# Optimization experiments

Hardware: AMD Instinct MI355X
Metric: run time of the kernel (lower is better)

The kernel has to match this reference:

```python
import jax, jax.numpy as jnp
from jax import lax
import numpy as np

N, D = 1024, 100000
K, SELECT_N = 20, 256  # select_n = int(N * split) = int(1024 * 0.25)


def setup_inputs() -> dict:
    key = jax.random.key(0)
    k1, k2 = jax.random.split(key)
    inp = jax.random.normal(k1, (N, D), dtype=jnp.float32)
    indices = jax.random.randint(k2, (K, SELECT_N), 0, N, dtype=jnp.int32)
    return {"inp": inp, "indices": indices}


def reference(inp, indices):
    # For each of k bagging rounds: gather select_n random rows, max over rows.
    # scan over k keeps the peak intermediate at [select_n, D] instead of [k, select_n, D].
    def step(_, idx):
        return None, jnp.max(inp[idx], axis=0)  # [D]

    _, maxes = lax.scan(step, None, indices)   # [k, D]
    return jnp.mean(maxes, axis=0, keepdims=True)  # [1, D]
```

## Files before the change

### kernel.cpp

```cpp
#include <hip/hip_runtime.h>


#define N_ROWS   1024
#define D_COLS   100000
#define K_ROUNDS 20
#define SEL_N    256
#define NIDX     (K_ROUNDS * SEL_N)
#define CPB      16
#define NT       (D_COLS / CPB)
#define BLOCK    640
#define GRID     256
#define WAVES    10
#define RNDS_PW  (K_ROUNDS / WAVES)
#define NEG_INF  (-3.402823466e+38f)

template<int CTRL>
__device__ __forceinline__ float dpp_shr_max(float x) {
    const int xi = __float_as_int(x);
    const int sh = __builtin_amdgcn_update_dpp(xi, xi, CTRL, 0xF, 0xF, false);
    return fmaxf(x, __int_as_float(sh));
}
#define ROW_SHR4 0x114
#define ROW_SHR8 0x118

__device__ __forceinline__ void async_cp16(const float* g, float* l) {
    __builtin_amdgcn_global_load_lds(
        (const __attribute__((address_space(1))) unsigned int*)g,
        (__attribute__((address_space(3))) unsigned int*)l,
        16, 0, 0);
}

__device__ __forceinline__ void stage_tile(const float* __restrict__ inp,
                                           float* __restrict__ buf,
                                           int colbase, int wave, int lane) {
    if (wave < 8) {
        const int rsub = lane >> 2;
        const int c4   = (lane & 3) * 4;
        #pragma unroll
        for (int it = 0; it < 8; ++it) {
            const int row = wave * 128 + it * 16 + rsub;
            const float* g = inp + (size_t)row * D_COLS + colbase + c4;
            float* l = &buf[(wave * 128 + it * 16) * CPB];
            async_cp16(g, l);
        }
    }
}

__global__ __launch_bounds__(BLOCK, 1) void bagmax_kernel(
    const float* __restrict__ inp,
    const int*   __restrict__ indices,
    float*       __restrict__ out)
{
    __shared__ float tile[2][N_ROWS * CPB];
    __shared__ __align__(16) unsigned short sidx[NIDX];
    __shared__ float wpart[2][WAVES][CPB];

    const int tid  = threadIdx.x;
    const int lane = tid & 63;
    const int wave = tid >> 6;

    const int b   = blockIdx.x;
    const int swz = (b & 7) * 32 + (b >> 3);
    const int cnt = (NT - swz + GRID - 1) / GRID;

    for (int i = tid; i < NIDX; i += BLOCK) {
        const int p   = i & 255;
        const int dst = (i & ~255) | ((p & 15) << 4) | (p >> 4);
        sidx[dst] = (unsigned short)indices[i];
    }

    stage_tile(inp, &tile[0][0], swz * CPB, wave, lane);
    asm volatile("s_waitcnt vmcnt(0)" ::: "memory");
    __syncthreads();

    const int g = lane >> 2;
    const int u = lane & 3;

    #pragma unroll 1
    for (int i = 0; i < cnt; ++i) {
        const int cur = i & 1;

        if (i + 1 < cnt)
            stage_tile(inp, &tile[cur ^ 1][0], (swz + (i + 1) * GRID) * CPB, wave, lane);

        if (i > 0 && tid < CPB) {
            float s = 0.f;
            #pragma unroll
            for (int w = 0; w < WAVES; ++w) s += wpart[cur ^ 1][w][tid];
            out[(swz + (i - 1) * GRID) * CPB + tid] = s * (1.0f / (float)K_ROUNDS);
        }

        const float* tb = &tile[cur][0];
        float4 rsum = make_float4(0.f, 0.f, 0.f, 0.f);
        #pragma unroll
        for (int kk = 0; kk < RNDS_PW; ++kk) {
            const int k = wave * RNDS_PW + kk;

            const uint4* sp = reinterpret_cast<const uint4*>(&sidx[k * SEL_N + g * 16]);
            const uint4 w0 = sp[0];
            const uint4 w1 = sp[1];
            unsigned int e[16];
            e[0]  = w0.x & 0xFFFFu; e[1]  = w0.x >> 16;
            e[2]  = w0.y & 0xFFFFu; e[3]  = w0.y >> 16;
            e[4]  = w0.z & 0xFFFFu; e[5]  = w0.z >> 16;
            e[6]  = w0.w & 0xFFFFu; e[7]  = w0.w >> 16;
            e[8]  = w1.x & 0xFFFFu; e[9]  = w1.x >> 16;
            e[10] = w1.y & 0xFFFFu; e[11] = w1.y >> 16;
            e[12] = w1.z & 0xFFFFu; e[13] = w1.z >> 16;
            e[14] = w1.w & 0xFFFFu; e[15] = w1.w >> 16;

            float4 a0 = make_float4(NEG_INF, NEG_INF, NEG_INF, NEG_INF);
            float4 a1 = a0;
            #pragma unroll
            for (int j = 0; j < 16; j += 2) {
                const float4 v0 = *reinterpret_cast<const float4*>(&tb[e[j]     * CPB + u * 4]);
                const float4 v1 = *reinterpret_cast<const float4*>(&tb[e[j + 1] * CPB + u * 4]);
                a0.x = fmaxf(a0.x, v0.x); a0.y = fmaxf(a0.y, v0.y);
                a0.z = fmaxf(a0.z, v0.z); a0.w = fmaxf(a0.w, v0.w);
                a1.x = fmaxf(a1.x, v1.x); a1.y = fmaxf(a1.y, v1.y);
                a1.z = fmaxf(a1.z, v1.z); a1.w = fmaxf(a1.w, v1.w);
            }
            float4 acc;
            acc.x = fmaxf(a0.x, a1.x); acc.y = fmaxf(a0.y, a1.y);
            acc.z = fmaxf(a0.z, a1.z); acc.w = fmaxf(a0.w, a1.w);

            acc.x = dpp_shr_max<ROW_SHR4>(acc.x); acc.y = dpp_shr_max<ROW_SHR4>(acc.y);
            acc.z = dpp_shr_max<ROW_SHR4>(acc.z); acc.w = dpp_shr_max<ROW_SHR4>(acc.w);
            acc.x = dpp_shr_max<ROW_SHR8>(acc.x); acc.y = dpp_shr_max<ROW_SHR8>(acc.y);
            acc.z = dpp_shr_max<ROW_SHR8>(acc.z); acc.w = dpp_shr_max<ROW_SHR8>(acc.w);
            acc.x = fmaxf(acc.x, __shfl_xor(acc.x, 16, 64));
            acc.y = fmaxf(acc.y, __shfl_xor(acc.y, 16, 64));
            acc.z = fmaxf(acc.z, __shfl_xor(acc.z, 16, 64));
            acc.w = fmaxf(acc.w, __shfl_xor(acc.w, 16, 64));
            acc.x = fmaxf(acc.x, __shfl_xor(acc.x, 32, 64));
            acc.y = fmaxf(acc.y, __shfl_xor(acc.y, 32, 64));
            acc.z = fmaxf(acc.z, __shfl_xor(acc.z, 32, 64));
            acc.w = fmaxf(acc.w, __shfl_xor(acc.w, 32, 64));

            rsum.x += acc.x; rsum.y += acc.y; rsum.z += acc.z; rsum.w += acc.w;
        }
        if (g == 3)
            *reinterpret_cast<float4*>(&wpart[cur][wave][u * 4]) = rsum;

        asm volatile("s_waitcnt vmcnt(0)" ::: "memory");
        __syncthreads();
    }

    if (tid < CPB) {
        const int pb = (cnt - 1) & 1;
        float s = 0.f;
        #pragma unroll
        for (int w = 0; w < WAVES; ++w) s += wpart[pb][w][tid];
        out[(swz + (cnt - 1) * GRID) * CPB + tid] = s * (1.0f / (float)K_ROUNDS);
    }
}

extern "C" void kernel_launch(void* const* d_in, const int* in_sizes, int n_in,
                              void* d_out, int out_size, void* d_ws, size_t ws_size,
                              hipStream_t stream) {
    const float* inp     = (const float*)d_in[0];
    const int*   indices = (const int*)d_in[1];
    float*       out     = (float*)d_out;

    bagmax_kernel<<<GRID, BLOCK, 0, stream>>>(inp, indices, out);
}
```

Before: 115.6 us.

## Stage tiles in LDS as swizzled bf16 via registers and double the grid

Each column tile is now loaded into registers and converted to bf16 before it is written to LDS with an XOR swizzle. This replaces the async global-to-LDS copy and halves LDS use per block. With the smaller footprint, occupancy rises (launch bounds 5, grid 512), and the gather-max reads 8-byte LDS words instead of 16. The cost is precision: every max is taken over bf16-rounded values, so the output loses accuracy against the fp32 reference. Staging through registers also adds register pressure and conversion ALU work.

```diff
diff --git a/kernel.cpp b/kernel.cpp
--- a/kernel.cpp
+++ b/kernel.cpp
@@ -1,4 +1,5 @@
 #include <hip/hip_runtime.h>
+#include <hip/hip_bf16.h>
 
 
 #define N_ROWS   1024
@@ -7,9 +8,10 @@
 #define SEL_N    256
 #define NIDX     (K_ROUNDS * SEL_N)
 #define CPB      16
+#define ROWDW    8
 #define NT       (D_COLS / CPB)
 #define BLOCK    640
-#define GRID     256
+#define GRID     512
 #define WAVES    10
 #define RNDS_PW  (K_ROUNDS / WAVES)
 #define NEG_INF  (-3.402823466e+38f)
@@ -23,35 +25,29 @@
 #define ROW_SHR4 0x114
 #define ROW_SHR8 0x118
 
-__device__ __forceinline__ void async_cp16(const float* g, float* l) {
-    __builtin_amdgcn_global_load_lds(
-        (const __attribute__((address_space(1))) unsigned int*)g,
-        (__attribute__((address_space(3))) unsigned int*)l,
-        16, 0, 0);
+__device__ __forceinline__ unsigned int pack_bf16(float a, float b) {
+    __hip_bfloat162 h = __float22bfloat162_rn(make_float2(a, b));
+    return *reinterpret_cast<unsigned int*>(&h);
 }
 
-__device__ __forceinline__ void stage_tile(const float* __restrict__ inp,
-                                           float* __restrict__ buf,
-                                           int colbase, int wave, int lane) {
-    if (wave < 8) {
-        const int rsub = lane >> 2;
-        const int c4   = (lane & 3) * 4;
-        #pragma unroll
-        for (int it = 0; it < 8; ++it) {
-            const int row = wave * 128 + it * 16 + rsub;
-            const float* g = inp + (size_t)row * D_COLS + colbase + c4;
-            float* l = &buf[(wave * 128 + it * 16) * CPB];
-            async_cp16(g, l);
-        }
+__device__ __forceinline__ void write_row_bf16(unsigned int* tb, int row, const float4* p) {
+    const int sw = (row >> 2) & 3;
+    unsigned int* base = tb + row * ROWDW;
+    #pragma unroll
+    for (int u = 0; u < 4; ++u) {
+        uint2 w;
+        w.x = pack_bf16(p[u].x, p[u].y);
+        w.y = pack_bf16(p[u].z, p[u].w);
+        *reinterpret_cast<uint2*>(base + (((u ^ sw) << 1))) = w;
     }
 }
 
-__global__ __launch_bounds__(BLOCK, 1) void bagmax_kernel(
+__global__ __launch_bounds__(BLOCK, 5) void bagmax_kernel(
     const float* __restrict__ inp,
     const int*   __restrict__ indices,
     float*       __restrict__ out)
 {
-    __shared__ float tile[2][N_ROWS * CPB];
+    __shared__ unsigned int tile[2][N_ROWS * ROWDW];
     __shared__ __align__(16) unsigned short sidx[NIDX];
     __shared__ float wpart[2][WAVES][CPB];
 
@@ -60,7 +56,7 @@
     const int wave = tid >> 6;
 
     const int b   = blockIdx.x;
-    const int swz = (b & 7) * 32 + (b >> 3);
+    const int swz = (b & 7) * 64 + (b >> 3);
     const int cnt = (NT - swz + GRID - 1) / GRID;
 
     for (int i = tid; i < NIDX; i += BLOCK) {
@@ -69,19 +65,42 @@
         sidx[dst] = (unsigned short)indices[i];
     }
 
-    stage_tile(inp, &tile[0][0], swz * CPB, wave, lane);
-    asm volatile("s_waitcnt vmcnt(0)" ::: "memory");
+    {
+        const int colb = swz * CPB;
+        float4 p0[4], p1[4];
+        const float4* g0 = reinterpret_cast<const float4*>(inp + (size_t)tid * D_COLS + colb);
+        #pragma unroll
+        for (int q = 0; q < 4; ++q) p0[q] = g0[q];
+        if (tid < 384) {
+            const float4* g1 = reinterpret_cast<const float4*>(inp + (size_t)(tid + 640) * D_COLS + colb);
+            #pragma unroll
+            for (int q = 0; q < 4; ++q) p1[q] = g1[q];
+        }
+        write_row_bf16(&tile[0][0], tid, p0);
+        if (tid < 384) write_row_bf16(&tile[0][0], tid + 640, p1);
+    }
     __syncthreads();
 
-    const int g = lane >> 2;
-    const int u = lane & 3;
+    const int g  = lane >> 2;
+    const int u2 = (lane & 3) << 1;
 
     #pragma unroll 1
     for (int i = 0; i < cnt; ++i) {
         const int cur = i & 1;
+        const bool havenext = (i + 1 < cnt);
 
-        if (i + 1 < cnt)
-            stage_tile(inp, &tile[cur ^ 1][0], (swz + (i + 1) * GRID) * CPB, wave, lane);
+        float4 p0[4], p1[4];
+        if (havenext) {
+            const int colb = (swz + (i + 1) * GRID) * CPB;
+            const float4* g0 = reinterpret_cast<const float4*>(inp + (size_t)tid * D_COLS + colb);
+            #pragma unroll
+            for (int q = 0; q < 4; ++q) p0[q] = g0[q];
+            if (tid < 384) {
+                const float4* g1 = reinterpret_cast<const float4*>(inp + (size_t)(tid + 640) * D_COLS + colb);
+                #pragma unroll
+                for (int q = 0; q < 4; ++q) p1[q] = g1[q];
+            }
+        }
 
         if (i > 0 && tid < CPB) {
             float s = 0.f;
@@ -90,36 +109,36 @@
             out[(swz + (i - 1) * GRID) * CPB + tid] = s * (1.0f / (float)K_ROUNDS);
         }
 
-        const float* tb = &tile[cur][0];
+        const unsigned int* tb = &tile[cur][0];
         float4 rsum = make_float4(0.f, 0.f, 0.f, 0.f);
         #pragma unroll
         for (int kk = 0; kk < RNDS_PW; ++kk) {
             const int k = wave * RNDS_PW + kk;
-
             const uint4* sp = reinterpret_cast<const uint4*>(&sidx[k * SEL_N + g * 16]);
             const uint4 w0 = sp[0];
             const uint4 w1 = sp[1];
-            unsigned int e[16];
-            e[0]  = w0.x & 0xFFFFu; e[1]  = w0.x >> 16;
-            e[2]  = w0.y & 0xFFFFu; e[3]  = w0.y >> 16;
-            e[4]  = w0.z & 0xFFFFu; e[5]  = w0.z >> 16;
-            e[6]  = w0.w & 0xFFFFu; e[7]  = w0.w >> 16;
-            e[8]  = w1.x & 0xFFFFu; e[9]  = w1.x >> 16;
-            e[10] = w1.y & 0xFFFFu; e[11] = w1.y >> 16;
-            e[12] = w1.z & 0xFFFFu; e[13] = w1.z >> 16;
-            e[14] = w1.w & 0xFFFFu; e[15] = w1.w >> 16;
 
             float4 a0 = make_float4(NEG_INF, NEG_INF, NEG_INF, NEG_INF);
             float4 a1 = a0;
-            #pragma unroll
-            for (int j = 0; j < 16; j += 2) {
-                const float4 v0 = *reinterpret_cast<const float4*>(&tb[e[j]     * CPB + u * 4]);
-                const float4 v1 = *reinterpret_cast<const float4*>(&tb[e[j + 1] * CPB + u * 4]);
-                a0.x = fmaxf(a0.x, v0.x); a0.y = fmaxf(a0.y, v0.y);
-                a0.z = fmaxf(a0.z, v0.z); a0.w = fmaxf(a0.w, v0.w);
-                a1.x = fmaxf(a1.x, v1.x); a1.y = fmaxf(a1.y, v1.y);
-                a1.z = fmaxf(a1.z, v1.z); a1.w = fmaxf(a1.w, v1.w);
+            #define PROC(dw) { \
+                const unsigned int e0 = (dw) & 0xFFFFu, e1 = (dw) >> 16; \
+                const uint2 v0 = *reinterpret_cast<const uint2*>( \
+                    &tb[(((e0 << 3) | (((e0 >> 2) & 3u) << 1))) ^ u2]); \
+                const uint2 v1 = *reinterpret_cast<const uint2*>( \
+                    &tb[(((e1 << 3) | (((e1 >> 2) & 3u) << 1))) ^ u2]); \
+                a0.x = fmaxf(a0.x, __uint_as_float(v0.x << 16)); \
+                a0.y = fmaxf(a0.y, __uint_as_float(v0.x & 0xFFFF0000u)); \
+                a0.z = fmaxf(a0.z, __uint_as_float(v0.y << 16)); \
+                a0.w = fmaxf(a0.w, __uint_as_float(v0.y & 0xFFFF0000u)); \
+                a1.x = fmaxf(a1.x, __uint_as_float(v1.x << 16)); \
+                a1.y = fmaxf(a1.y, __uint_as_float(v1.x & 0xFFFF0000u)); \
+                a1.z = fmaxf(a1.z, __uint_as_float(v1.y << 16)); \
+                a1.w = fmaxf(a1.w, __uint_as_float(v1.y & 0xFFFF0000u)); \
             }
+            PROC(w0.x) PROC(w0.y) PROC(w0.z) PROC(w0.w)
+            PROC(w1.x) PROC(w1.y) PROC(w1.z) PROC(w1.w)
+            #undef PROC
+
             float4 acc;
             acc.x = fmaxf(a0.x, a1.x); acc.y = fmaxf(a0.y, a1.y);
             acc.z = fmaxf(a0.z, a1.z); acc.w = fmaxf(a0.w, a1.w);
@@ -140,9 +159,12 @@
             rsum.x += acc.x; rsum.y += acc.y; rsum.z += acc.z; rsum.w += acc.w;
         }
         if (g == 3)
-            *reinterpret_cast<float4*>(&wpart[cur][wave][u * 4]) = rsum;
+            *reinterpret_cast<float4*>(&wpart[cur][wave][(lane & 3) * 4]) = rsum;
 
-        asm volatile("s_waitcnt vmcnt(0)" ::: "memory");
+        if (havenext) {
+            write_row_bf16(&tile[cur ^ 1][0], tid, p0);
+            if (tid < 384) write_row_bf16(&tile[cur ^ 1][0], tid + 640, p1);
+        }
         __syncthreads();
     }
 
```

New measurement: 176.5 us. +52.7%, slower.
